# Kernel optimization log

Measured on AMD Instinct MI355X. Metric: run time of the kernel, lower is better.

The kernel has to match this reference:

```python
import jax, jax.numpy as jnp
import numpy as np

DEPTH = 4
NUM_INTERNAL = 2 ** DEPTH - 1  # 15
NUM_LEAVES = 2 ** DEPTH        # 16
INPUT_DIM = 1024
NUM_CLASSES = 100
LEAF_HIDDEN = 256
BATCH = 4096
TAU = 1.0
EPS = 1e-10


def setup_inputs() -> dict:
    key = jax.random.key(0)
    ks = jax.random.split(key, 8)
    x = jax.random.normal(ks[0], (BATCH, INPUT_DIM), dtype=jnp.float32)
    gumbel_u = jax.random.uniform(ks[1], (NUM_INTERNAL, BATCH, INPUT_DIM), dtype=jnp.float32)
    feature_logits = jax.random.normal(ks[2], (NUM_INTERNAL, INPUT_DIM), dtype=jnp.float32) * 0.1
    split_thresholds = jnp.zeros((NUM_INTERNAL,), dtype=jnp.float32)
    feature_weights = jax.random.normal(ks[3], (NUM_INTERNAL, INPUT_DIM), dtype=jnp.float32) / np.sqrt(INPUT_DIM)
    # leaf MLPs, kaiming-normal init (fan_in), zero bias
    W1 = jax.random.normal(ks[4], (NUM_LEAVES, LEAF_HIDDEN, INPUT_DIM), dtype=jnp.float32) * np.sqrt(2.0 / INPUT_DIM)
    b1 = jnp.zeros((NUM_LEAVES, LEAF_HIDDEN), dtype=jnp.float32)
    W2 = jax.random.normal(ks[5], (NUM_LEAVES, NUM_CLASSES, LEAF_HIDDEN), dtype=jnp.float32) * np.sqrt(2.0 / LEAF_HIDDEN)
    b2 = jnp.zeros((NUM_LEAVES, NUM_CLASSES), dtype=jnp.float32)
    return {
        'x': x, 'gumbel_u': gumbel_u,
        'feature_logits': feature_logits, 'split_thresholds': split_thresholds,
        'feature_weights': feature_weights, 'W1': W1, 'b1': b1, 'W2': W2, 'b2': b2,
    }


def reference(x, gumbel_u, feature_logits, split_thresholds, feature_weights, W1, b1, W2, b2):
    # --- Gumbel-softmax feature gating (soft, tau=TAU) for ALL nodes at once ---
    g = -jnp.log(-jnp.log(gumbel_u + EPS) + EPS)                 # [N, B, D]
    imp = jax.nn.softmax((feature_logits[:, None, :] + g) / TAU, axis=-1)  # [N, B, D]
    # aggregated split value: sum_d x * importance * feature_weight
    agg = jnp.einsum('bd,nbd,nd->nb', x, imp, feature_weights)   # [N, B]
    split_prob = jax.nn.sigmoid((agg - split_thresholds[:, None]) / TAU)   # [N, B]

    # --- leaf routing probabilities (level-order traversal) ---
    probs = jnp.ones((1, x.shape[0]), dtype=x.dtype)             # [1, B]
    for level in range(DEPTH):
        n = 2 ** level
        s = jax.lax.dynamic_slice_in_dim(split_prob, n - 1, n, axis=0)  # [n, B]
        # order per node: left then right -> interleave
        probs = jnp.stack([probs * (1.0 - s), probs * s], axis=1).reshape(2 * n, -1)
    leaf_probs = probs                                           # [L, B]

    # --- leaf MLPs (dropout is identity in eval), batched over leaves ---
    h = jax.nn.relu(jnp.einsum('bd,lhd->lbh', x, W1) + b1[:, None, :])      # [L, B, H]
    leaf_out = jnp.einsum('lbh,lch->lbc', h, W2) + b2[:, None, :]           # [L, B, C]

    # weighted combine over leaves
    logits = jnp.einsum('lbc,lb->bc', leaf_out, leaf_probs)     # [B, C]
    return logits
```

## Files before the change

kernel.cpp:

```cpp
#include <hip/hip_runtime.h>
#include <hip/hip_bf16.h>
#include <cstdint>
#include <cstddef>

#define NI 15
#define NL 16
#define DD 1024
#define NC 100
#define HH 256
#define BB 4096

typedef __attribute__((ext_vector_type(8))) short bf16x8;
typedef __attribute__((ext_vector_type(8))) unsigned short u16x8;
typedef __attribute__((ext_vector_type(4))) float f32x4;

__device__ __forceinline__ unsigned short f2bf(float f) {
  union { float f; unsigned u; } v; v.f = f;
  return (unsigned short)((v.u + 0x7FFFu + ((v.u >> 16) & 1u)) >> 16);
}

__device__ __forceinline__ void gld_lds16(const void* g, void* s) {
  __builtin_amdgcn_global_load_lds(
      (const __attribute__((address_space(1))) unsigned int*)g,
      (__attribute__((address_space(3))) unsigned int*)s, 16, 0, 0);
}

__global__ __launch_bounds__(256) void k_convert(const float* __restrict__ src,
                                                 unsigned short* __restrict__ dst,
                                                 int n) {
  const int stride = gridDim.x * blockDim.x * 4;
  for (int i = (blockIdx.x * blockDim.x + threadIdx.x) * 4; i < n; i += stride) {
    float4 v = *reinterpret_cast<const float4*>(src + i);
    ushort4 o;
    o.x = f2bf(v.x); o.y = f2bf(v.y); o.z = f2bf(v.z); o.w = f2bf(v.w);
    *reinterpret_cast<ushort4*>(dst + i) = o;
  }
}

__global__ __launch_bounds__(256) void k_gate(
    const float* __restrict__ x, const float* __restrict__ gu,
    const float* __restrict__ fl, const float* __restrict__ thr,
    const float* __restrict__ fw, float* __restrict__ split) {
  const int b = blockIdx.x;
  const int w = threadIdx.x >> 6, lane = threadIdx.x & 63;
  const int d0 = lane * 16;

  float xr[16];
  {
    const float* xp = x + (size_t)b * DD + d0;
    for (int j = 0; j < 4; ++j) {
      float4 v = *reinterpret_cast<const float4*>(xp + j * 4);
      xr[j * 4 + 0] = v.x; xr[j * 4 + 1] = v.y;
      xr[j * 4 + 2] = v.z; xr[j * 4 + 3] = v.w;
    }
  }

  for (int n = w; n < NI; n += 4) {
    const float* gp = gu + ((size_t)n * BB + b) * DD + d0;
    const float* fp = fl + (size_t)n * DD + d0;
    const float* wp = fw + (size_t)n * DD + d0;
    float num = 0.f, den = 0.f;
    for (int j = 0; j < 4; ++j) {
      float4 g4 = *reinterpret_cast<const float4*>(gp + j * 4);
      float4 f4 = *reinterpret_cast<const float4*>(fp + j * 4);
      float4 w4 = *reinterpret_cast<const float4*>(wp + j * 4);
      float gv[4] = {g4.x, g4.y, g4.z, g4.w};
      float fv[4] = {f4.x, f4.y, f4.z, f4.w};
      float wv[4] = {w4.x, w4.y, w4.z, w4.w};
      for (int q = 0; q < 4; ++q) {
        float gg = -__logf(-__logf(gv[q] + 1e-10f) + 1e-10f);
        float e = __expf(fv[q] + gg);
        den += e;
        num += xr[j * 4 + q] * wv[q] * e;
      }
    }
    for (int off = 32; off; off >>= 1) {
      num += __shfl_xor(num, off);
      den += __shfl_xor(den, off);
    }
    if (lane == 0) {
      float agg = num / den;
      split[n * BB + b] = 1.f / (1.f + __expf(-(agg - thr[n])));
    }
  }
}

__global__ __launch_bounds__(256) void k_leaf(const float* __restrict__ split,
                                              float* __restrict__ lp) {
  const int b = blockIdx.x * blockDim.x + threadIdx.x;
  if (b >= BB) return;
  float s[NI];
  for (int i = 0; i < NI; ++i) s[i] = split[i * BB + b];
  for (int leaf = 0; leaf < NL; ++leaf) {
    float p = 1.f;
    int node = 0;
    for (int lev = 0; lev < 4; ++lev) {
      int bit = (leaf >> (3 - lev)) & 1;
      p *= bit ? s[node] : (1.f - s[node]);
      node = 2 * node + 1 + bit;
    }
    lp[(size_t)b * NL + leaf] = p;
  }
}

__global__ __launch_bounds__(256) void k_gemm1(
    const unsigned short* __restrict__ xb, const unsigned short* __restrict__ w1b,
    const float* __restrict__ b1, const float* __restrict__ lp,
    unsigned short* __restrict__ hs) {
  __shared__ unsigned short lA[128 * 64];
  __shared__ unsigned short lB[128 * 64];
  __shared__ float s_lp[128];
  __shared__ float s_b1[128];

  const int tid = threadIdx.x;
  const int mt = blockIdx.x, nt = blockIdx.y, l = blockIdx.z;
  const int m0 = mt * 128, n0 = nt * 128;

  if (tid < 128) s_lp[tid] = lp[(size_t)(m0 + tid) * NL + l];
  else           s_b1[tid - 128] = b1[l * HH + n0 + (tid - 128)];

  const unsigned short* Ag = xb + (size_t)m0 * DD;
  const unsigned short* Bg = w1b + (size_t)l * HH * DD + (size_t)n0 * DD;

  f32x4 acc[4][4] = {};
  const int wv = tid >> 6, lane = tid & 63;
  const int wm = (wv & 1) * 64, wn = (wv >> 1) * 64;
  const int fr = lane & 15, fk = (lane >> 4) * 8;
  const int srow = tid >> 3, scol = (tid & 7) * 8;

  for (int k0 = 0; k0 < DD; k0 += 64) {
    for (int i = 0; i < 4; ++i)
      gld_lds16(Ag + (size_t)(srow + i * 32) * DD + k0 + scol,
                &lA[(srow + i * 32) * 64 + scol]);
    for (int i = 0; i < 4; ++i)
      gld_lds16(Bg + (size_t)(srow + i * 32) * DD + k0 + scol,
                &lB[(srow + i * 32) * 64 + scol]);
    __syncthreads();
    for (int kk = 0; kk < 64; kk += 32) {
      bf16x8 av[4], bv[4];
      for (int i = 0; i < 4; ++i)
        av[i] = *reinterpret_cast<const bf16x8*>(&lA[(wm + i * 16 + fr) * 64 + kk + fk]);
      for (int i = 0; i < 4; ++i)
        bv[i] = *reinterpret_cast<const bf16x8*>(&lB[(wn + i * 16 + fr) * 64 + kk + fk]);
      for (int mi = 0; mi < 4; ++mi)
        for (int ni = 0; ni < 4; ++ni)
          acc[mi][ni] = __builtin_amdgcn_mfma_f32_16x16x32_bf16(av[mi], bv[ni], acc[mi][ni], 0, 0, 0);
    }
    __syncthreads();
  }

  const int cr = (lane >> 4) * 4, cc = lane & 15;
  for (int mi = 0; mi < 4; ++mi)
    for (int ni = 0; ni < 4; ++ni) {
      const int col = wn + ni * 16 + cc;
      const float bias = s_b1[col];
      for (int j = 0; j < 4; ++j) {
        const int row = wm + mi * 16 + cr + j;
        float v = acc[mi][ni][j] + bias;
        v = fmaxf(v, 0.f) * s_lp[row];
        hs[(size_t)l * BB * HH + (size_t)(m0 + row) * HH + (n0 + col)] = f2bf(v);
      }
    }
}

__global__ __launch_bounds__(256) void k_gemm2(
    const unsigned short* __restrict__ hs, const unsigned short* __restrict__ w2b,
    const float* __restrict__ b2, const float* __restrict__ lp,
    float* __restrict__ out) {
  __shared__ unsigned short lA[128 * 64];
  __shared__ unsigned short lB[128 * 64];
  __shared__ float s_lp[128 * NL];

  const int tid = threadIdx.x;
  const int mt = blockIdx.x, kc = blockIdx.y;
  const int m0 = mt * 128;

  {
    const float4* src = reinterpret_cast<const float4*>(lp + (size_t)m0 * NL);
    reinterpret_cast<float4*>(s_lp)[tid * 2 + 0] = src[tid * 2 + 0];
    reinterpret_cast<float4*>(s_lp)[tid * 2 + 1] = src[tid * 2 + 1];
  }

  f32x4 acc[4][4] = {};
  const int wv = tid >> 6, lane = tid & 63;
  const int wm = (wv & 1) * 64, wn = (wv >> 1) * 64;
  const int fr = lane & 15, fk = (lane >> 4) * 8;
  const int srow = tid >> 3, scol = (tid & 7) * 8;

  for (int ks = 0; ks < 8; ++ks) {
    const int kg = kc * 512 + ks * 64;
    const int l = kg >> 8, h0 = kg & 255;
    const unsigned short* Ag = hs + (size_t)l * BB * HH + (size_t)m0 * HH + h0;
    for (int i = 0; i < 4; ++i)
      gld_lds16(Ag + (size_t)(srow + i * 32) * HH + scol,
                &lA[(srow + i * 32) * 64 + scol]);
    const unsigned short* Bg = w2b + (size_t)l * NC * HH + h0;
    for (int i = 0; i < 4; ++i) {
      const int c = srow + i * 32;
      u16x8 v = {};
      if (c < NC) v = *reinterpret_cast<const u16x8*>(Bg + (size_t)c * HH + scol);
      *reinterpret_cast<u16x8*>(&lB[c * 64 + scol]) = v;
    }
    __syncthreads();
    for (int kk = 0; kk < 64; kk += 32) {
      bf16x8 av[4], bv[4];
      for (int i = 0; i < 4; ++i)
        av[i] = *reinterpret_cast<const bf16x8*>(&lA[(wm + i * 16 + fr) * 64 + kk + fk]);
      for (int i = 0; i < 4; ++i)
        bv[i] = *reinterpret_cast<const bf16x8*>(&lB[(wn + i * 16 + fr) * 64 + kk + fk]);
      for (int mi = 0; mi < 4; ++mi)
        for (int ni = 0; ni < 4; ++ni)
          acc[mi][ni] = __builtin_amdgcn_mfma_f32_16x16x32_bf16(av[mi], bv[ni], acc[mi][ni], 0, 0, 0);
    }
    __syncthreads();
  }

  const int cr = (lane >> 4) * 4, cc = lane & 15;
  for (int mi = 0; mi < 4; ++mi)
    for (int ni = 0; ni < 4; ++ni) {
      const int col = wn + ni * 16 + cc;
      if (col < NC) {
        for (int j = 0; j < 4; ++j) {
          const int row = wm + mi * 16 + cr + j;
          float v = acc[mi][ni][j];
          if (kc == 0) {
            float bias = 0.f;
            for (int q = 0; q < NL; ++q) bias += s_lp[row * NL + q] * b2[q * NC + col];
            v += bias;
          }
          atomicAdd(&out[(size_t)(m0 + row) * NC + col], v);
        }
      }
    }
}

extern "C" void kernel_launch(void* const* d_in, const int* in_sizes, int n_in,
                              void* d_out, int out_size, void* d_ws, size_t ws_size,
                              hipStream_t stream) {
  const float* x   = (const float*)d_in[0];
  const float* gu  = (const float*)d_in[1];
  const float* fl  = (const float*)d_in[2];
  const float* thr = (const float*)d_in[3];
  const float* fw  = (const float*)d_in[4];
  const float* W1  = (const float*)d_in[5];
  const float* b1  = (const float*)d_in[6];
  const float* W2  = (const float*)d_in[7];
  const float* b2  = (const float*)d_in[8];
  float* out = (float*)d_out;

  char* ws = (char*)d_ws;
  float* split          = (float*)(ws + 0);
  float* lp             = (float*)(ws + 245760);
  unsigned short* xb    = (unsigned short*)(ws + 507904);
  unsigned short* w1b   = (unsigned short*)(ws + 8896512);
  unsigned short* w2b   = (unsigned short*)(ws + 17285120);
  unsigned short* hsb   = (unsigned short*)(ws + 18104320);

  k_convert<<<2048, 256, 0, stream>>>(x,  xb,  BB * DD);
  k_convert<<<2048, 256, 0, stream>>>(W1, w1b, NL * HH * DD);
  k_convert<<<512,  256, 0, stream>>>(W2, w2b, NL * NC * HH);

  k_gate<<<BB, 256, 0, stream>>>(x, gu, fl, thr, fw, split);
  k_leaf<<<16, 256, 0, stream>>>(split, lp);

  k_gemm1<<<dim3(32, 2, 16), 256, 0, stream>>>(xb, w1b, b1, lp, hsb);

  hipMemsetAsync(out, 0, (size_t)out_size * sizeof(float), stream);
  k_gemm2<<<dim3(32, 8, 1), 256, 0, stream>>>(hsb, w2b, b2, lp, out);
}
```

Before: 557.0 us.

## Fuse x bf16 conversion into gate kernel and replace atomics with split-K reduce

Result: faster. 472.5 us (-15.2%).

```diff
diff --git a/kernel.cpp b/kernel.cpp
--- a/kernel.cpp
+++ b/kernel.cpp
@@ -40,38 +40,45 @@
 __global__ __launch_bounds__(256) void k_gate(
     const float* __restrict__ x, const float* __restrict__ gu,
     const float* __restrict__ fl, const float* __restrict__ thr,
-    const float* __restrict__ fw, float* __restrict__ split) {
+    const float* __restrict__ fw, float* __restrict__ split,
+    unsigned short* __restrict__ xb) {
   const int b = blockIdx.x;
   const int w = threadIdx.x >> 6, lane = threadIdx.x & 63;
-  const int d0 = lane * 16;
 
   float xr[16];
-  {
-    const float* xp = x + (size_t)b * DD + d0;
+  const float* xp = x + (size_t)b * DD;
+  for (int j = 0; j < 4; ++j) {
+    float4 v = *reinterpret_cast<const float4*>(xp + lane * 4 + j * 256);
+    xr[j * 4 + 0] = v.x; xr[j * 4 + 1] = v.y;
+    xr[j * 4 + 2] = v.z; xr[j * 4 + 3] = v.w;
+  }
+  if (w == 0) {
     for (int j = 0; j < 4; ++j) {
-      float4 v = *reinterpret_cast<const float4*>(xp + j * 4);
-      xr[j * 4 + 0] = v.x; xr[j * 4 + 1] = v.y;
-      xr[j * 4 + 2] = v.z; xr[j * 4 + 3] = v.w;
+      ushort4 o;
+      o.x = f2bf(xr[j * 4 + 0]); o.y = f2bf(xr[j * 4 + 1]);
+      o.z = f2bf(xr[j * 4 + 2]); o.w = f2bf(xr[j * 4 + 3]);
+      *reinterpret_cast<ushort4*>(xb + (size_t)b * DD + lane * 4 + j * 256) = o;
     }
   }
 
   for (int n = w; n < NI; n += 4) {
-    const float* gp = gu + ((size_t)n * BB + b) * DD + d0;
-    const float* fp = fl + (size_t)n * DD + d0;
-    const float* wp = fw + (size_t)n * DD + d0;
+    const float* gp = gu + ((size_t)n * BB + b) * DD;
+    const float* fp = fl + (size_t)n * DD;
+    const float* wp = fw + (size_t)n * DD;
     float num = 0.f, den = 0.f;
     for (int j = 0; j < 4; ++j) {
-      float4 g4 = *reinterpret_cast<const float4*>(gp + j * 4);
-      float4 f4 = *reinterpret_cast<const float4*>(fp + j * 4);
-      float4 w4 = *reinterpret_cast<const float4*>(wp + j * 4);
+      const int e = lane * 4 + j * 256;
+      float4 g4 = *reinterpret_cast<const float4*>(gp + e);
+      float4 f4 = *reinterpret_cast<const float4*>(fp + e);
+      float4 w4 = *reinterpret_cast<const float4*>(wp + e);
       float gv[4] = {g4.x, g4.y, g4.z, g4.w};
       float fv[4] = {f4.x, f4.y, f4.z, f4.w};
       float wv[4] = {w4.x, w4.y, w4.z, w4.w};
       for (int q = 0; q < 4; ++q) {
         float gg = -__logf(-__logf(gv[q] + 1e-10f) + 1e-10f);
-        float e = __expf(fv[q] + gg);
-        den += e;
-        num += xr[j * 4 + q] * wv[q] * e;
+        float e2 = __expf(fv[q] + gg);
+        den += e2;
+        num += xr[j * 4 + q] * wv[q] * e2;
       }
     }
     for (int off = 32; off; off >>= 1) {
@@ -165,21 +172,13 @@
 
 __global__ __launch_bounds__(256) void k_gemm2(
     const unsigned short* __restrict__ hs, const unsigned short* __restrict__ w2b,
-    const float* __restrict__ b2, const float* __restrict__ lp,
-    float* __restrict__ out) {
+    float* __restrict__ part) {
   __shared__ unsigned short lA[128 * 64];
   __shared__ unsigned short lB[128 * 64];
-  __shared__ float s_lp[128 * NL];
 
   const int tid = threadIdx.x;
   const int mt = blockIdx.x, kc = blockIdx.y;
   const int m0 = mt * 128;
-
-  {
-    const float4* src = reinterpret_cast<const float4*>(lp + (size_t)m0 * NL);
-    reinterpret_cast<float4*>(s_lp)[tid * 2 + 0] = src[tid * 2 + 0];
-    reinterpret_cast<float4*>(s_lp)[tid * 2 + 1] = src[tid * 2 + 1];
-  }
 
   f32x4 acc[4][4] = {};
   const int wv = tid >> 6, lane = tid & 63;
@@ -222,16 +221,24 @@
       if (col < NC) {
         for (int j = 0; j < 4; ++j) {
           const int row = wm + mi * 16 + cr + j;
-          float v = acc[mi][ni][j];
-          if (kc == 0) {
-            float bias = 0.f;
-            for (int q = 0; q < NL; ++q) bias += s_lp[row * NL + q] * b2[q * NC + col];
-            v += bias;
-          }
-          atomicAdd(&out[(size_t)(m0 + row) * NC + col], v);
+          part[((size_t)kc * BB + m0 + row) * NC + col] = acc[mi][ni][j];
         }
       }
     }
+}
+
+__global__ __launch_bounds__(256) void k_reduce(const float* __restrict__ part,
+                                                const float* __restrict__ lp,
+                                                const float* __restrict__ b2,
+                                                float* __restrict__ out) {
+  const int i = blockIdx.x * 256 + threadIdx.x;
+  if (i >= BB * NC) return;
+  const int b = i / NC, c = i - b * NC;
+  float v = 0.f;
+  for (int k = 0; k < 8; ++k) v += part[(size_t)k * BB * NC + i];
+  const float* lpp = lp + (size_t)b * NL;
+  for (int l = 0; l < NL; ++l) v += lpp[l] * b2[l * NC + c];
+  out[i] = v;
 }
 
 extern "C" void kernel_launch(void* const* d_in, const int* in_sizes, int n_in,
@@ -255,16 +262,14 @@
   unsigned short* w1b   = (unsigned short*)(ws + 8896512);
   unsigned short* w2b   = (unsigned short*)(ws + 17285120);
   unsigned short* hsb   = (unsigned short*)(ws + 18104320);
-
-  k_convert<<<2048, 256, 0, stream>>>(x,  xb,  BB * DD);
+  float* part           = (float*)(ws + 51658752);
+
+  k_gate<<<BB, 256, 0, stream>>>(x, gu, fl, thr, fw, split, xb);
   k_convert<<<2048, 256, 0, stream>>>(W1, w1b, NL * HH * DD);
   k_convert<<<512,  256, 0, stream>>>(W2, w2b, NL * NC * HH);
-
-  k_gate<<<BB, 256, 0, stream>>>(x, gu, fl, thr, fw, split);
   k_leaf<<<16, 256, 0, stream>>>(split, lp);
 
   k_gemm1<<<dim3(32, 2, 16), 256, 0, stream>>>(xb, w1b, b1, lp, hsb);
-
-  hipMemsetAsync(out, 0, (size_t)out_size * sizeof(float), stream);
-  k_gemm2<<<dim3(32, 8, 1), 256, 0, stream>>>(hsb, w2b, b2, lp, out);
-}
+  k_gemm2<<<dim3(32, 8, 1), 256, 0, stream>>>(hsb, w2b, part);
+  k_reduce<<<1600, 256, 0, stream>>>(part, lp, b2, out);
+}
```
